# Optimization experiments

Measured on AMD Instinct MI355X. Metric: run time of the kernel, lower is better.

The kernel has to match this reference:

```python
import jax, jax.numpy as jnp
import numpy as np

HEAD_SIZE = 64
BLOCK_SIZE = 4096
BATCH = 4


def setup_inputs() -> dict:
    key = jax.random.key(0)
    kx, kk, kq, kv = jax.random.split(key, 4)
    x = jax.random.normal(kx, (BATCH, BLOCK_SIZE, HEAD_SIZE), dtype=jnp.float32)
    s = HEAD_SIZE ** -0.5  # ~ torch default linear init scale
    Wk = jax.random.uniform(kk, (HEAD_SIZE, HEAD_SIZE), jnp.float32, -s, s)
    Wq = jax.random.uniform(kq, (HEAD_SIZE, HEAD_SIZE), jnp.float32, -s, s)
    Wv = jax.random.uniform(kv, (HEAD_SIZE, HEAD_SIZE), jnp.float32, -s, s)
    return {"x": x, "Wk": Wk, "Wq": Wq, "Wv": Wv}


def reference(x, Wk, Wq, Wv):
    # x: [B, T, C]; W*: [C, C] stored torch-style (out, in) -> y = x @ W.T
    B, T, C = x.shape
    k = x @ Wk.T  # [B, T, C]
    q = x @ Wq.T
    v = x @ Wv.T
    scores = jnp.einsum('btc,bsc->bts', q, k) * (C ** -0.5)  # [B, T, T]
    causal = jnp.tril(jnp.ones((T, T), dtype=bool))
    scores = jnp.where(causal, scores, -jnp.inf)
    weights = jax.nn.softmax(scores, axis=-1)
    out = jnp.einsum('bts,bsc->btc', weights, v)  # [B, T, C]
    return out
```

## Files before the change

kernel.cpp:

```cpp
#include <hip/hip_runtime.h>
#include <hip/hip_bf16.h>

typedef unsigned short u16;
typedef unsigned int u32;
typedef __bf16 bf16x8_t __attribute__((ext_vector_type(8)));
typedef float f32x4_t __attribute__((ext_vector_type(4)));
typedef float f32x16 __attribute__((ext_vector_type(16)));

constexpr int Bb = 4;
constexpr int Tt = 4096;
constexpr int Dd = 64;
constexpr float QSCALE = 0.18033688011112042f;

__device__ __forceinline__ u16 f2bf(float f) {
  unsigned int u = __builtin_bit_cast(unsigned int, f);
  return (u16)((u + 0x7fffu + ((u >> 16) & 1u)) >> 16);
}
__device__ __forceinline__ u32 pk2(float a, float b) {
  return (u32)f2bf(a) | ((u32)f2bf(b) << 16);
}
__device__ __forceinline__ u32 pkt(float a, float b) {
  const u32 ua = __builtin_bit_cast(u32, a);
  const u32 ub = __builtin_bit_cast(u32, b);
  return (ua >> 16) | (ub & 0xFFFF0000u);
}
__device__ __forceinline__ bf16x8_t ld16(const u16* p) {
  int4 v = *(const int4*)p;
  return __builtin_bit_cast(bf16x8_t, v);
}
__device__ __forceinline__ f32x4_t mfma16(bf16x8_t a, bf16x8_t b, f32x4_t c) {
  return __builtin_amdgcn_mfma_f32_16x16x32_bf16(a, b, c, 0, 0, 0);
}
__device__ __forceinline__ f32x16 mfma32(bf16x8_t a, bf16x8_t b, f32x16 c) {
  return __builtin_amdgcn_mfma_f32_32x32x16_bf16(a, b, c, 0, 0, 0);
}

__global__ __launch_bounds__(1024) void HeadV1_proj(
    const float* __restrict__ x, const float* __restrict__ Wk,
    const float* __restrict__ Wq, const float* __restrict__ Wv,
    u16* __restrict__ qS, u16* __restrict__ kS, u16* __restrict__ vS)
{
  __shared__ u16 xl[64][72];
  __shared__ u16 Wl[3][64][72];
  __shared__ u16 yl[3][64][72];

  const int t = threadIdx.x;
  const int w = t >> 6, lane = t & 63, l15 = lane & 15, quad = lane >> 4;
  const int blk = blockIdx.x;
  const int r0 = blk * 64;
  const int b  = blk >> 6;
  const int kt = blk & 63;
  const long tilebase = ((long)(b * 64 + kt)) * 4096;

  {
    const float* srcs[4] = {x + (long)r0 * 64, Wk, Wq, Wv};
    u16* dstl[4] = {&xl[0][0], &Wl[0][0][0], &Wl[1][0][0], &Wl[2][0][0]};
    const int row = t >> 4, c4 = t & 15;
    #pragma unroll
    for (int mm = 0; mm < 4; mm++) {
      float4 v = ((const float4*)(srcs[mm] + row * 64))[c4];
      uint2 pk;
      pk.x = pk2(v.x, v.y);
      pk.y = pk2(v.z, v.w);
      *(uint2*)(dstl[mm] + row * 72 + c4 * 4) = pk;
    }
  }
  __syncthreads();

  const int mg = w >> 2;
  const int wl = w & 3;
  if (mg < 3) {
    bf16x8_t xf[2];
    #pragma unroll
    for (int kh = 0; kh < 2; kh++)
      xf[kh] = ld16(&xl[wl * 16 + l15][kh * 32 + quad * 8]);

    float vals[4][4];
    #pragma unroll
    for (int g = 0; g < 4; g++) {
      f32x4_t acc = {0.f, 0.f, 0.f, 0.f};
      #pragma unroll
      for (int kh = 0; kh < 2; kh++) {
        bf16x8_t wf = ld16(&Wl[mg][g * 16 + l15][kh * 32 + quad * 8]);
        acc = mfma16(xf[kh], wf, acc);
      }
      #pragma unroll
      for (int r = 0; r < 4; r++)
        vals[g][r] = (mg == 1) ? acc[r] * QSCALE : acc[r];
    }
    #pragma unroll
    for (int g = 0; g < 4; g++)
      #pragma unroll
      for (int r = 0; r < 4; r++)
        yl[mg][wl * 16 + quad * 4 + r][g * 16 + l15] = f2bf(vals[g][r]);
  }
  __syncthreads();

  if (mg < 3) {
    u16* dsts[3];
    dsts[0] = kS + tilebase; dsts[1] = qS + tilebase; dsts[2] = vS + tilebase;
    if (mg < 2) {
      #pragma unroll
      for (int kk = 0; kk < 2; kk++) {
        bf16x8_t f = ld16(&yl[mg][wl * 16 + l15][kk * 32 + quad * 8]);
        *(int4*)(dsts[mg] + (wl * 2 + kk) * 512 + lane * 8) = __builtin_bit_cast(int4, f);
      }
    } else {
      #pragma unroll
      for (int kk = 0; kk < 2; kk++) {
        u16 tmp[8];
        #pragma unroll
        for (int jj = 0; jj < 8; jj++)
          tmp[jj] = yl[2][kk * 32 + quad * 8 + jj][wl * 16 + l15];
        *(int4*)(dsts[2] + (kk * 4 + wl) * 512 + lane * 8) = *(const int4*)tmp;
      }
    }
  }
}

__global__ __launch_bounds__(1024, 4) void HeadV1_flash(
    const u16* __restrict__ qS, const u16* __restrict__ kS,
    const u16* __restrict__ vS, float* __restrict__ outg)
{
  __shared__ __align__(16) char smem[55296];
  float (*chk)[16][33]  = (float (*)[16][33])smem;
  float (*stg)[32][68]  = (float (*)[32][68])(smem + 33792);
  float (*lst)[2][32]   = (float (*)[2][32])(smem + 51200);

  const int t    = threadIdx.x;
  const int w    = t >> 6;
  const int lane = t & 63;
  const int l15  = lane & 15;
  const int lhb  = lane >> 5;
  const int l4   = (lane >> 4) & 1;
  const int q31  = lane & 31;

  const int xcd = blockIdx.x & 7;
  const int b   = xcd >> 1;
  const int i   = ((blockIdx.x >> 3) << 1) | (xcd & 1);
  const int j1 = i, j2 = 127 - i;
  const int nk1 = (j1 >> 1) + 1;
  const int nk2 = (j2 >> 1) + 1;
  int n1 = (16 * nk1 + 32) / 65;
  if (n1 < 1) n1 = 1;
  if (n1 > 15) n1 = 15;

  const bool grp2 = (w >= n1);
  const int j   = grp2 ? j2 : j1;
  const int nk  = grp2 ? nk2 : nk1;
  const int str = grp2 ? (16 - n1) : n1;
  const int off = grp2 ? (w - n1) : w;

  const int qt64 = j >> 1;
  const int ql0  = (j & 1) * 32;
  const int qr0  = j * 32;
  const long base = (long)b * Tt * Dd;

  union { u32 u4[4]; bf16x8_t v; } uo;
  uo.u4[0] = uo.u4[1] = uo.u4[2] = uo.u4[3] = 0x3F803F80u;
  const bf16x8_t ones = uo.v;

  const u16* qt_ = qS + ((long)(b * 64 + qt64)) * 4096;
  bf16x8_t qfrag[4];
  #pragma unroll
  for (int dsl = 0; dsl < 4; dsl++)
    qfrag[dsl] = ld16(qt_ + (((ql0 >> 4) + l4) * 2 + (dsl >> 1)) * 512
                          + (((dsl * 2 + lhb) & 3) * 16 + l15) * 8);

  f32x16 O0 = {0.f,0.f,0.f,0.f,0.f,0.f,0.f,0.f,0.f,0.f,0.f,0.f,0.f,0.f,0.f,0.f};
  f32x16 O1 = O0;
  f32x16 Lacc = O0;

  const u16* kb = kS + ((long)(b * 64)) * 4096;
  const u16* vb = vS + ((long)(b * 64)) * 4096;

  for (int kt = off; kt < nk; kt += str) {
    const bool ismask = (kt == nk - 1);
    const u16* ktile = kb + (long)kt * 4096;
    const u16* vtile = vb + (long)kt * 4096;
    const int nh = (ismask && !(j & 1)) ? 1 : 2;

    for (int h2 = 0; h2 < nh; h2++) {
      bf16x8_t kf[4];
      #pragma unroll
      for (int dsl = 0; dsl < 4; dsl++)
        kf[dsl] = ld16(ktile + ((h2 * 2 + l4) * 2 + (dsl >> 1)) * 512
                             + (((dsl * 2 + lhb) & 3) * 16 + l15) * 8);
      bf16x8_t vf[2][2];
      #pragma unroll
      for (int ksl = 0; ksl < 2; ksl++)
        #pragma unroll
        for (int dh = 0; dh < 2; dh++)
          vf[ksl][dh] = ld16(vtile + (h2 * 4 + dh * 2 + l4) * 512
                                   + ((ksl * 2 + lhb) * 16 + l15) * 8);

      f32x16 S = {0.f,0.f,0.f,0.f,0.f,0.f,0.f,0.f,0.f,0.f,0.f,0.f,0.f,0.f,0.f,0.f};
      #pragma unroll
      for (int dsl = 0; dsl < 4; dsl++)
        S = mfma32(kf[dsl], qfrag[dsl], S);

      if (ismask && h2 == (j & 1)) {
        const int kvb = kt * 64 + h2 * 32 + 4 * lhb;
        const int qi  = qr0 + q31;
        #pragma unroll
        for (int r = 0; r < 16; r++) {
          const int kvg = kvb + (r & 3) + 8 * (r >> 2);
          if (kvg > qi) S[r] = -1e30f;
        }
      }

      #pragma unroll
      for (int ksl = 0; ksl < 2; ksl++) {
        const u32 a0 = pkt(__builtin_amdgcn_exp2f(S[8 * ksl + 0]),
                           __builtin_amdgcn_exp2f(S[8 * ksl + 1]));
        const u32 a1 = pkt(__builtin_amdgcn_exp2f(S[8 * ksl + 2]),
                           __builtin_amdgcn_exp2f(S[8 * ksl + 3]));
        const u32 a2 = pkt(__builtin_amdgcn_exp2f(S[8 * ksl + 4]),
                           __builtin_amdgcn_exp2f(S[8 * ksl + 5]));
        const u32 a3 = pkt(__builtin_amdgcn_exp2f(S[8 * ksl + 6]),
                           __builtin_amdgcn_exp2f(S[8 * ksl + 7]));
        const u32 x02 = (u32)__shfl_xor((int)(lhb ? a0 : a2), 32);
        const u32 x13 = (u32)__shfl_xor((int)(lhb ? a1 : a3), 32);
        uint4 bw;
        bw.x = lhb ? x02 : a0;
        bw.y = lhb ? x13 : a1;
        bw.z = lhb ? a2 : x02;
        bw.w = lhb ? a3 : x13;
        const bf16x8_t Bf = __builtin_bit_cast(bf16x8_t, bw);
        Lacc = mfma32(ones, Bf, Lacc);
        __builtin_amdgcn_s_setprio(1);
        O0 = mfma32(vf[ksl][0], Bf, O0);
        O1 = mfma32(vf[ksl][1], Bf, O1);
        __builtin_amdgcn_s_setprio(0);
      }
    }
  }

  lst[w][lhb][q31] = Lacc[0];
  __syncthreads();

  #pragma unroll
  for (int rr = 0; rr < 4; rr++) {
    #pragma unroll
    for (int rs = 0; rs < 8; rs++) {
      const int dloc = (rs & 3) + 8 * (rs >> 2) + 4 * lhb;
      const float val = (rr >> 1) ? ((rr & 1) ? O1[8 + rs] : O1[rs])
                                  : ((rr & 1) ? O0[8 + rs] : O0[rs]);
      chk[w][dloc][q31] = val;
    }
    __syncthreads();
    {
      const int jsel = t >> 9, tt = t & 511;
      const int d2 = tt >> 5, q = tt & 31;
      const int lo = jsel ? n1 : 0, hi = jsel ? 16 : n1;
      float s = 0.f;
      for (int w2 = lo; w2 < hi; w2++) s += chk[w2][d2][q];
      stg[jsel][q][rr * 16 + d2] = s;
    }
    __syncthreads();
  }

  {
    const int jsel = t >> 9, tt = t & 511;
    const int q = tt >> 4, dg = tt & 15;
    const int lo = jsel ? n1 : 0, hi = jsel ? 16 : n1;
    float L = 0.f;
    for (int w2 = lo; w2 < hi; w2++) L += lst[w2][0][q];
    const float invL = 1.0f / L;
    const int jj = jsel ? j2 : j1;
    float4 v = *(const float4*)&stg[jsel][q][dg * 4];
    v.x *= invL; v.y *= invL; v.z *= invL; v.w *= invL;
    *(float4*)(outg + base + (long)(jj * 32 + q) * 64 + dg * 4) = v;
  }
}

extern "C" void kernel_launch(void* const* d_in, const int* in_sizes, int n_in,
                              void* d_out, int out_size, void* d_ws, size_t ws_size,
                              hipStream_t stream) {
  (void)in_sizes; (void)n_in; (void)out_size; (void)ws_size;
  const float* x  = (const float*)d_in[0];
  const float* Wk = (const float*)d_in[1];
  const float* Wq = (const float*)d_in[2];
  const float* Wv = (const float*)d_in[3];
  float* out = (float*)d_out;
  u16* qw  = (u16*)d_ws;
  u16* kw  = qw + (size_t)Bb * Tt * Dd;
  u16* vw  = kw + (size_t)Bb * Tt * Dd;

  HeadV1_proj<<<(Bb * Tt) / 64, 1024, 0, stream>>>(x, Wk, Wq, Wv, qw, kw, vw);
  HeadV1_flash<<<256, 1024, 0, stream>>>(qw, kw, vw, out);
}
```

Baseline: 82.92 us.

## Process one 64-row query tile per block with Q staged in LDS

Each block now handles a single 64-row query tile instead of a balanced pair of 32-row tiles. Q is staged in LDS, so each K/V fragment load feeds two 32-row score blocks. The softmax row sums are now accumulated on the VALU with truncated values rather than through an MFMA against ones. This drops the causal load-balancing pairing, so blocks near the diagonal end carry very unequal work. It also raises LDS use and removes the occupancy hint from the launch bounds.

```diff
diff --git a/kernel.cpp b/kernel.cpp
--- a/kernel.cpp
+++ b/kernel.cpp
@@ -118,14 +118,15 @@
   }
 }
 
-__global__ __launch_bounds__(1024, 4) void HeadV1_flash(
+__global__ __launch_bounds__(1024) void HeadV1_flash(
     const u16* __restrict__ qS, const u16* __restrict__ kS,
     const u16* __restrict__ vS, float* __restrict__ outg)
 {
-  __shared__ __align__(16) char smem[55296];
-  float (*chk)[16][33]  = (float (*)[16][33])smem;
-  float (*stg)[32][68]  = (float (*)[32][68])(smem + 33792);
-  float (*lst)[2][32]   = (float (*)[2][32])(smem + 51200);
+  __shared__ __align__(16) char smem[93184];
+  u16*  qlds            = (u16*)smem;
+  float (*chk)[16][66]  = (float (*)[16][66])smem;
+  float (*stg)[32][68]  = (float (*)[32][68])(smem + 67584);
+  float (*lst)[2][2][32]= (float (*)[2][2][32])(smem + 84992);
 
   const int t    = threadIdx.x;
   const int w    = t >> 6;
@@ -138,54 +139,88 @@
   const int xcd = blockIdx.x & 7;
   const int b   = xcd >> 1;
   const int i   = ((blockIdx.x >> 3) << 1) | (xcd & 1);
-  const int j1 = i, j2 = 127 - i;
-  const int nk1 = (j1 >> 1) + 1;
-  const int nk2 = (j2 >> 1) + 1;
-  int n1 = (16 * nk1 + 32) / 65;
-  if (n1 < 1) n1 = 1;
-  if (n1 > 15) n1 = 15;
-
-  const bool grp2 = (w >= n1);
-  const int j   = grp2 ? j2 : j1;
-  const int nk  = grp2 ? nk2 : nk1;
-  const int str = grp2 ? (16 - n1) : n1;
-  const int off = grp2 ? (w - n1) : w;
-
-  const int qt64 = j >> 1;
-  const int ql0  = (j & 1) * 32;
-  const int qr0  = j * 32;
+  const int nk  = i + 1;
   const long base = (long)b * Tt * Dd;
 
-  union { u32 u4[4]; bf16x8_t v; } uo;
-  uo.u4[0] = uo.u4[1] = uo.u4[2] = uo.u4[3] = 0x3F803F80u;
-  const bf16x8_t ones = uo.v;
-
-  const u16* qt_ = qS + ((long)(b * 64 + qt64)) * 4096;
-  bf16x8_t qfrag[4];
-  #pragma unroll
-  for (int dsl = 0; dsl < 4; dsl++)
-    qfrag[dsl] = ld16(qt_ + (((ql0 >> 4) + l4) * 2 + (dsl >> 1)) * 512
-                          + (((dsl * 2 + lhb) & 3) * 16 + l15) * 8);
-
-  f32x16 O0 = {0.f,0.f,0.f,0.f,0.f,0.f,0.f,0.f,0.f,0.f,0.f,0.f,0.f,0.f,0.f,0.f};
-  f32x16 O1 = O0;
-  f32x16 Lacc = O0;
+  {
+    const u16* qt_ = qS + ((long)(b * 64 + i)) * 4096;
+    *(int4*)(qlds + t * 8) = *(const int4*)(qt_ + t * 8);
+  }
+  __syncthreads();
+
+  const f32x16 z16 = {0.f,0.f,0.f,0.f,0.f,0.f,0.f,0.f,0.f,0.f,0.f,0.f,0.f,0.f,0.f,0.f};
+  f32x16 OA0 = z16, OA1 = z16, OB0 = z16, OB1 = z16;
+  float LpA = 0.f, LpB = 0.f;
 
   const u16* kb = kS + ((long)(b * 64)) * 4096;
   const u16* vb = vS + ((long)(b * 64)) * 4096;
 
-  for (int kt = off; kt < nk; kt += str) {
-    const bool ismask = (kt == nk - 1);
+  auto tr = [](float e) {
+    return __builtin_bit_cast(float, __builtin_bit_cast(u32, e) & 0xFFFF0000u);
+  };
+  auto packhalf = [&](const f32x16& S, int ksl, float& Lp) -> bf16x8_t {
+    const float e0 = __builtin_amdgcn_exp2f(S[8 * ksl + 0]);
+    const float e1 = __builtin_amdgcn_exp2f(S[8 * ksl + 1]);
+    const float e2 = __builtin_amdgcn_exp2f(S[8 * ksl + 2]);
+    const float e3 = __builtin_amdgcn_exp2f(S[8 * ksl + 3]);
+    const float e4 = __builtin_amdgcn_exp2f(S[8 * ksl + 4]);
+    const float e5 = __builtin_amdgcn_exp2f(S[8 * ksl + 5]);
+    const float e6 = __builtin_amdgcn_exp2f(S[8 * ksl + 6]);
+    const float e7 = __builtin_amdgcn_exp2f(S[8 * ksl + 7]);
+    Lp += ((tr(e0) + tr(e1)) + (tr(e2) + tr(e3))) + ((tr(e4) + tr(e5)) + (tr(e6) + tr(e7)));
+    const u32 b0 = pkt(e0, e1), b1 = pkt(e2, e3), b2 = pkt(e4, e5), b3 = pkt(e6, e7);
+    const u32 x02 = (u32)__shfl_xor((int)(lhb ? b0 : b2), 32);
+    const u32 x13 = (u32)__shfl_xor((int)(lhb ? b1 : b3), 32);
+    uint4 bw;
+    bw.x = lhb ? x02 : b0;
+    bw.y = lhb ? x13 : b1;
+    bw.z = lhb ? b2 : x02;
+    bw.w = lhb ? b3 : x13;
+    return __builtin_bit_cast(bf16x8_t, bw);
+  };
+
+  for (int kt = w; kt < nk; kt += 16) {
+    const bool last = (kt == nk - 1);
     const u16* ktile = kb + (long)kt * 4096;
     const u16* vtile = vb + (long)kt * 4096;
-    const int nh = (ismask && !(j & 1)) ? 1 : 2;
-
-    for (int h2 = 0; h2 < nh; h2++) {
+
+    #pragma unroll
+    for (int h2 = 0; h2 < 2; h2++) {
+      const bool doA = !(last && h2 == 1);
+
       bf16x8_t kf[4];
       #pragma unroll
       for (int dsl = 0; dsl < 4; dsl++)
         kf[dsl] = ld16(ktile + ((h2 * 2 + l4) * 2 + (dsl >> 1)) * 512
                              + (((dsl * 2 + lhb) & 3) * 16 + l15) * 8);
+
+      bf16x8_t BfA0, BfA1;
+      if (doA) {
+        f32x16 S = z16;
+        #pragma unroll
+        for (int dsl = 0; dsl < 4; dsl++)
+          S = mfma32(kf[dsl], ld16(qlds + (l4 * 2 + (dsl >> 1)) * 512
+                                        + (((dsl * 2 + lhb) & 3) * 16 + l15) * 8), S);
+        if (last) {
+          #pragma unroll
+          for (int r = 0; r < 16; r++)
+            if (4 * lhb + (r & 3) + 8 * (r >> 2) > q31) S[r] = -1e30f;
+        }
+        BfA0 = packhalf(S, 0, LpA);
+        BfA1 = packhalf(S, 1, LpA);
+      }
+
+      f32x16 S = z16;
+      #pragma unroll
+      for (int dsl = 0; dsl < 4; dsl++)
+        S = mfma32(kf[dsl], ld16(qlds + ((2 + l4) * 2 + (dsl >> 1)) * 512
+                                      + (((dsl * 2 + lhb) & 3) * 16 + l15) * 8), S);
+      if (last && h2 == 1) {
+        #pragma unroll
+        for (int r = 0; r < 16; r++)
+          if (4 * lhb + (r & 3) + 8 * (r >> 2) > q31) S[r] = -1e30f;
+      }
+
       bf16x8_t vf[2][2];
       #pragma unroll
       for (int ksl = 0; ksl < 2; ksl++)
@@ -194,49 +229,22 @@
           vf[ksl][dh] = ld16(vtile + (h2 * 4 + dh * 2 + l4) * 512
                                    + ((ksl * 2 + lhb) * 16 + l15) * 8);
 
-      f32x16 S = {0.f,0.f,0.f,0.f,0.f,0.f,0.f,0.f,0.f,0.f,0.f,0.f,0.f,0.f,0.f,0.f};
-      #pragma unroll
-      for (int dsl = 0; dsl < 4; dsl++)
-        S = mfma32(kf[dsl], qfrag[dsl], S);
-
-      if (ismask && h2 == (j & 1)) {
-        const int kvb = kt * 64 + h2 * 32 + 4 * lhb;
-        const int qi  = qr0 + q31;
-        #pragma unroll
-        for (int r = 0; r < 16; r++) {
-          const int kvg = kvb + (r & 3) + 8 * (r >> 2);
-          if (kvg > qi) S[r] = -1e30f;
-        }
-      }
-
-      #pragma unroll
-      for (int ksl = 0; ksl < 2; ksl++) {
-        const u32 a0 = pkt(__builtin_amdgcn_exp2f(S[8 * ksl + 0]),
-                           __builtin_amdgcn_exp2f(S[8 * ksl + 1]));
-        const u32 a1 = pkt(__builtin_amdgcn_exp2f(S[8 * ksl + 2]),
-                           __builtin_amdgcn_exp2f(S[8 * ksl + 3]));
-        const u32 a2 = pkt(__builtin_amdgcn_exp2f(S[8 * ksl + 4]),
-                           __builtin_amdgcn_exp2f(S[8 * ksl + 5]));
-        const u32 a3 = pkt(__builtin_amdgcn_exp2f(S[8 * ksl + 6]),
-                           __builtin_amdgcn_exp2f(S[8 * ksl + 7]));
-        const u32 x02 = (u32)__shfl_xor((int)(lhb ? a0 : a2), 32);
-        const u32 x13 = (u32)__shfl_xor((int)(lhb ? a1 : a3), 32);
-        uint4 bw;
-        bw.x = lhb ? x02 : a0;
-        bw.y = lhb ? x13 : a1;
-        bw.z = lhb ? a2 : x02;
-        bw.w = lhb ? a3 : x13;
-        const bf16x8_t Bf = __builtin_bit_cast(bf16x8_t, bw);
-        Lacc = mfma32(ones, Bf, Lacc);
-        __builtin_amdgcn_s_setprio(1);
-        O0 = mfma32(vf[ksl][0], Bf, O0);
-        O1 = mfma32(vf[ksl][1], Bf, O1);
-        __builtin_amdgcn_s_setprio(0);
-      }
-    }
-  }
-
-  lst[w][lhb][q31] = Lacc[0];
+      const bf16x8_t BfB0 = packhalf(S, 0, LpB);
+      const bf16x8_t BfB1 = packhalf(S, 1, LpB);
+
+      __builtin_amdgcn_s_setprio(1);
+      if (doA) {
+        OA0 = mfma32(vf[0][0], BfA0, OA0);  OA1 = mfma32(vf[0][1], BfA0, OA1);
+        OA0 = mfma32(vf[1][0], BfA1, OA0);  OA1 = mfma32(vf[1][1], BfA1, OA1);
+      }
+      OB0 = mfma32(vf[0][0], BfB0, OB0);  OB1 = mfma32(vf[0][1], BfB0, OB1);
+      OB0 = mfma32(vf[1][0], BfB1, OB0);  OB1 = mfma32(vf[1][1], BfB1, OB1);
+      __builtin_amdgcn_s_setprio(0);
+    }
+  }
+
+  lst[w][0][lhb][q31] = LpA;
+  lst[w][1][lhb][q31] = LpB;
   __syncthreads();
 
   #pragma unroll
@@ -244,33 +252,34 @@
     #pragma unroll
     for (int rs = 0; rs < 8; rs++) {
       const int dloc = (rs & 3) + 8 * (rs >> 2) + 4 * lhb;
-      const float val = (rr >> 1) ? ((rr & 1) ? O1[8 + rs] : O1[rs])
-                                  : ((rr & 1) ? O0[8 + rs] : O0[rs]);
-      chk[w][dloc][q31] = val;
+      const float vA = (rr >> 1) ? ((rr & 1) ? OA1[8 + rs] : OA1[rs])
+                                 : ((rr & 1) ? OA0[8 + rs] : OA0[rs]);
+      const float vB = (rr >> 1) ? ((rr & 1) ? OB1[8 + rs] : OB1[rs])
+                                 : ((rr & 1) ? OB0[8 + rs] : OB0[rs]);
+      chk[w][dloc][q31]      = vA;
+      chk[w][dloc][32 + q31] = vB;
     }
     __syncthreads();
     {
-      const int jsel = t >> 9, tt = t & 511;
-      const int d2 = tt >> 5, q = tt & 31;
-      const int lo = jsel ? n1 : 0, hi = jsel ? 16 : n1;
+      const int d2 = t >> 6, q = t & 63;
       float s = 0.f;
-      for (int w2 = lo; w2 < hi; w2++) s += chk[w2][d2][q];
-      stg[jsel][q][rr * 16 + d2] = s;
+      #pragma unroll
+      for (int w2 = 0; w2 < 16; w2++) s += chk[w2][d2][q];
+      stg[q >> 5][q & 31][rr * 16 + d2] = s;
     }
     __syncthreads();
   }
 
   {
-    const int jsel = t >> 9, tt = t & 511;
+    const int g = t >> 9, tt = t & 511;
     const int q = tt >> 4, dg = tt & 15;
-    const int lo = jsel ? n1 : 0, hi = jsel ? 16 : n1;
     float L = 0.f;
-    for (int w2 = lo; w2 < hi; w2++) L += lst[w2][0][q];
+    #pragma unroll
+    for (int w2 = 0; w2 < 16; w2++) L += lst[w2][g][0][q] + lst[w2][g][1][q];
     const float invL = 1.0f / L;
-    const int jj = jsel ? j2 : j1;
-    float4 v = *(const float4*)&stg[jsel][q][dg * 4];
+    float4 v = *(const float4*)&stg[g][q][dg * 4];
     v.x *= invL; v.y *= invL; v.z *= invL; v.w *= invL;
-    *(float4*)(outg + base + (long)(jj * 32 + q) * 64 + dg * 4) = v;
+    *(float4*)(outg + base + (long)(i * 64 + g * 32 + q) * 64 + dg * 4) = v;
   }
 }
 
```

Result: slower. 125.3 us (+51.1%).
